# Performance work log

Hardware: AMD Instinct MI355X
Metric: run time of the kernel (lower is better)

Reference implementation:

```python
import jax, jax.numpy as jnp
import numpy as np

L = 64          # chain length
D = 16          # bond dimension
S = 2           # local (spin) dimension
N = 131072      # batch of spin configurations


def setup_inputs() -> dict:
    key = jax.random.key(0)
    k1, k2, k3, k4 = jax.random.split(key, 4)
    scale = 1.0 / np.sqrt(D * S)  # matches init_tensors normal_(0, 1/sqrt(D*S))
    left = jax.random.normal(k1, (1, D, S), dtype=jnp.float32) * scale
    bulk = jax.random.normal(k2, (D, D, S), dtype=jnp.float32) * scale
    right = jax.random.normal(k3, (D, 1, S), dtype=jnp.float32) * scale
    x = jax.random.randint(k4, (N, L), 0, S)
    return {"x": x, "left": left, "bulk": bulk, "right": right}


def reference(x, left, bulk, right):
    # x: (N, L) int spins; amplitude(x) -> (N,)
    n, l = x.shape
    # left (1,D,S): gather left matrix per sample -> (N, D) (row vector, left bond is 1)
    leftT = left[0].T                      # (S, D)
    m0 = leftT[x[:, 0]]                    # (N, D)
    bulkT = jnp.transpose(bulk, (2, 0, 1))  # (S, D, D)
    xs = x[:, 1:l - 1].T                   # (L-2, N) bulk-site spins

    def step(m, s):
        # m: (N, D), bulkT[s]: (N, D, D) -> batched vec-mat product
        return jnp.einsum('nd,nde->ne', m, bulkT[s]), None

    m, _ = jax.lax.scan(step, m0, xs)      # (N, D)
    rightT = jnp.transpose(right, (2, 0, 1))[:, :, 0]  # (S, D)
    a = jnp.einsum('nd,nd->n', m, rightT[x[:, l - 1]])  # (N,)
    return a
```

## Files before the change

### kernel.cpp

```cpp
#include <hip/hip_runtime.h>

#define OFF_V    0u
#define OFF_W    262144u
#define OFF_P    524288u
#define OFF_VA   1048576u
#define OFF_WB   1050624u
#define OFF_PAV  1052672u
#define OFF_PAW  1085440u
#define OFF_PC0  1118208u
#define OFF_PC1  1150976u
#define OFF_PACK 1167360u

__device__ __forceinline__ void rmul16(float* v, const float* B) {
  float nv[16];
#pragma unroll
  for (int e = 0; e < 16; ++e) {
    float a = 0.f;
#pragma unroll
    for (int d = 0; d < 16; ++d) a = fmaf(v[d], B[d * 16 + e], a);
    nv[e] = a;
  }
#pragma unroll
  for (int e = 0; e < 16; ++e) v[e] = nv[e];
}

__device__ __forceinline__ void lmul16(float* v, const float* B) {
  float nv[16];
#pragma unroll
  for (int d = 0; d < 16; ++d) {
    float a = 0.f;
#pragma unroll
    for (int e = 0; e < 16; ++e) a = fmaf(B[d * 16 + e], v[e], a);
    nv[d] = a;
  }
#pragma unroll
  for (int d = 0; d < 16; ++d) v[d] = nv[d];
}

__global__ __launch_bounds__(256) void build_a(const float* __restrict__ left,
                                               const float* __restrict__ bulk,
                                               const float* __restrict__ right,
                                               const int* __restrict__ x,
                                               float* __restrict__ ws) {
  int tid = threadIdx.x;

  if (blockIdx.x >= 29) {
    int lane = tid & 63;
    int wave = tid >> 6;
    unsigned pb = blockIdx.x - 29;
    unsigned seqbase = pb * 256u + wave * 64u;
    const int* __restrict__ xp = x + (size_t)seqbase * 64;
    unsigned long long word = 0ull;
#pragma unroll
    for (int rb = 0; rb < 8; ++rb) {
      int vals[8];
#pragma unroll
      for (int j = 0; j < 8; ++j) vals[j] = xp[(size_t)(rb * 8 + j) * 64 + lane];
#pragma unroll
      for (int j = 0; j < 8; ++j) {
        unsigned long long mm = __ballot(vals[j] & 1);
        if (lane == rb * 8 + j) word = mm;
      }
    }
    reinterpret_cast<unsigned long long*>(ws + OFF_PACK)[seqbase + lane] = word;
    return;
  }

  __shared__ float Bs[2][256];
  __shared__ float Ls[2][16];
  __shared__ float Rs[2][16];
  for (int i = tid; i < 576; i += 256) {
    if (i < 512) Bs[i & 1][i >> 1] = bulk[i];
    else if (i < 544) { int j = i - 512; Ls[j & 1][j >> 1] = left[j]; }
    else              { int j = i - 544; Rs[j & 1][j >> 1] = right[j]; }
  }
  __syncthreads();

  unsigned gid = blockIdx.x * 256 + tid;
  float v[16];
  if (gid < 128) {
    unsigned i = gid;
#pragma unroll
    for (int d = 0; d < 16; ++d) v[d] = Ls[i & 1][d];
    for (int t = 1; t <= 6; ++t) rmul16(v, Bs[(i >> t) & 1]);
#pragma unroll
    for (int d = 0; d < 16; ++d) ws[OFF_VA + i * 16 + d] = v[d];
  } else if (gid < 256) {
    unsigned i = gid - 128;
#pragma unroll
    for (int d = 0; d < 16; ++d) v[d] = Rs[(i >> 6) & 1][d];
    for (int p = 5; p >= 0; --p) lmul16(v, Bs[(i >> p) & 1]);
#pragma unroll
    for (int d = 0; d < 16; ++d) ws[OFF_WB + i * 16 + d] = v[d];
  } else if (gid < 2304) {
    unsigned it = gid - 256, i = it >> 4, col = it & 15;
#pragma unroll
    for (int d = 0; d < 16; ++d) v[d] = Bs[(i >> 6) & 1][d * 16 + col];
    for (int p = 5; p >= 0; --p) lmul16(v, Bs[(i >> p) & 1]);
#pragma unroll
    for (int d = 0; d < 16; ++d) ws[OFF_PAV + i * 256 + d * 16 + col] = v[d];
  } else if (gid < 4352) {
    unsigned it = gid - 2304, i = it >> 4, col = it & 15;
#pragma unroll
    for (int d = 0; d < 16; ++d) v[d] = Bs[(i >> 6) & 1][d * 16 + col];
    for (int p = 5; p >= 0; --p) lmul16(v, Bs[(i >> p) & 1]);
#pragma unroll
    for (int d = 0; d < 16; ++d) ws[OFF_PAW + i * 256 + d * 16 + col] = v[d];
  } else {
    unsigned it = gid - 4352, c = it / 768, r = it - c * 768;
    if (r < 512) {
      unsigned i = r >> 4, col = r & 15;
#pragma unroll
      for (int d = 0; d < 16; ++d) v[d] = Bs[(i >> 4) & 1][d * 16 + col];
      for (int p = 3; p >= 0; --p) lmul16(v, Bs[(i >> p) & 1]);
#pragma unroll
      for (int d = 0; d < 16; ++d) ws[OFF_PC0 + c * 8192 + i * 256 + d * 16 + col] = v[d];
    } else {
      unsigned r2 = r - 512, i = r2 >> 4, col = r2 & 15;
#pragma unroll
      for (int d = 0; d < 16; ++d) v[d] = Bs[(i >> 3) & 1][d * 16 + col];
      for (int p = 2; p >= 0; --p) lmul16(v, Bs[(i >> p) & 1]);
#pragma unroll
      for (int d = 0; d < 16; ++d) ws[OFF_PC1 + c * 4096 + i * 256 + d * 16 + col] = v[d];
    }
  }
}

__global__ __launch_bounds__(256) void build_b(float* __restrict__ ws) {
  unsigned gid = blockIdx.x * 256 + threadIdx.x;
  if (gid < 262144u) {
    unsigned i = gid >> 4, e = gid & 15;
    const float* va = ws + OFF_VA + (i & 127) * 16;
    const float* pm = ws + OFF_PAV + (i >> 7) * 256;
    float a = 0.f;
#pragma unroll
    for (int k = 0; k < 16; ++k) a = fmaf(va[k], pm[k * 16 + e], a);
    ws[OFF_V + (size_t)i * 16 + e] = a;
  } else if (gid < 524288u) {
    unsigned g = gid - 262144u, i = g >> 4, d = g & 15;
    const float* wb = ws + OFF_WB + (i >> 7) * 16;
    const float* pm = ws + OFF_PAW + (i & 127) * 256 + d * 16;
    float a = 0.f;
#pragma unroll
    for (int k = 0; k < 16; ++k) a = fmaf(pm[k], wb[k], a);
    ws[OFF_W + (size_t)i * 16 + d] = a;
  } else {
    unsigned g = gid - 524288u;
    unsigned c = g >> 17, rem = g & 131071u;
    unsigned idx = rem >> 8, d = (rem >> 4) & 15, e = rem & 15;
    const float* p0 = ws + OFF_PC0 + c * 8192 + (idx & 31) * 256 + d * 16;
    const float* p1 = ws + OFF_PC1 + c * 4096 + (idx >> 5) * 256 + e;
    float a = 0.f;
#pragma unroll
    for (int k = 0; k < 16; ++k) a = fmaf(p0[k], p1[k * 16], a);
    ws[OFF_P + ((size_t)c << 17) + (size_t)idx * 256 + d * 16 + e] = a;
  }
}

__global__ __launch_bounds__(256, 4) void mps_main(const float* __restrict__ ws,
                                                   float* __restrict__ out) {
  __shared__ float sm[4][4][16];
  const int tid = threadIdx.x;
  const int lane = tid & 63;
  const int wave = tid >> 6;
  const int grp = lane >> 4;
  const int e = lane & 15;
  const unsigned seqw = blockIdx.x * 16u + wave * 4u;

  unsigned long long bits =
      reinterpret_cast<const unsigned long long*>(ws + OFF_PACK)[seqw + grp];

  const unsigned i0 = (unsigned)(bits & 0x3FFFull);
  const unsigned iw = (unsigned)(bits >> 50);
  unsigned idx0 = (unsigned)((bits >> 14) & 511ull);
  unsigned idx1 = (unsigned)((bits >> 23) & 511ull);
  unsigned idx2 = (unsigned)((bits >> 32) & 511ull);
  unsigned idx3 = (unsigned)((bits >> 41) & 511ull);

  float mv = ws[OFF_V + (size_t)i0 * 16 + e];
  float w  = ws[OFF_W + (size_t)iw * 16 + e];

  const float* __restrict__ P0 = ws + OFF_P;
  float p[4][16];
  {
    const float* pb = P0 + (size_t)idx0 * 256 + e;
#pragma unroll
    for (int d = 0; d < 16; ++d) p[0][d] = pb[d * 16];
  }
  {
    const float* pb = P0 + (1u << 17) + (size_t)idx1 * 256 + e;
#pragma unroll
    for (int d = 0; d < 16; ++d) p[1][d] = pb[d * 16];
  }
  {
    const float* pb = P0 + (2u << 17) + (size_t)idx2 * 256 + e;
#pragma unroll
    for (int d = 0; d < 16; ++d) p[2][d] = pb[d * 16];
  }
  {
    const float* pb = P0 + (3u << 17) + (size_t)idx3 * 256 + e;
#pragma unroll
    for (int d = 0; d < 16; ++d) p[3][d] = pb[d * 16];
  }

#pragma unroll
  for (int ch = 0; ch < 4; ++ch) {
    sm[wave][grp][e] = mv;
    asm volatile("" ::: "memory");
    float4 M0 = *(const float4*)&sm[wave][grp][0];
    float4 M1 = *(const float4*)&sm[wave][grp][4];
    float4 M2 = *(const float4*)&sm[wave][grp][8];
    float4 M3 = *(const float4*)&sm[wave][grp][12];
    asm volatile("" ::: "memory");
    float a0 = M0.x * p[ch][0];
    float a1 = M0.y * p[ch][1];
    float a2 = M0.z * p[ch][2];
    float a3 = M0.w * p[ch][3];
    a0 = fmaf(M1.x, p[ch][4], a0);
    a1 = fmaf(M1.y, p[ch][5], a1);
    a2 = fmaf(M1.z, p[ch][6], a2);
    a3 = fmaf(M1.w, p[ch][7], a3);
    a0 = fmaf(M2.x, p[ch][8], a0);
    a1 = fmaf(M2.y, p[ch][9], a1);
    a2 = fmaf(M2.z, p[ch][10], a2);
    a3 = fmaf(M2.w, p[ch][11], a3);
    a0 = fmaf(M3.x, p[ch][12], a0);
    a1 = fmaf(M3.y, p[ch][13], a1);
    a2 = fmaf(M3.z, p[ch][14], a2);
    a3 = fmaf(M3.w, p[ch][15], a3);
    mv = (a0 + a1) + (a2 + a3);
  }

  float part = mv * w;
  part += __shfl_xor(part, 1, 64);
  part += __shfl_xor(part, 2, 64);
  part += __shfl_xor(part, 4, 64);
  part += __shfl_xor(part, 8, 64);
  if (e == 0) out[seqw + grp] = part;
}

extern "C" void kernel_launch(void* const* d_in, const int* in_sizes, int n_in,
                              void* d_out, int out_size, void* d_ws, size_t ws_size,
                              hipStream_t stream) {
  const int* x = (const int*)d_in[0];
  const float* left = (const float*)d_in[1];
  const float* bulk = (const float*)d_in[2];
  const float* right = (const float*)d_in[3];
  float* out = (float*)d_out;
  float* ws = (float*)d_ws;

  int nseq = in_sizes[0] / 64;

  build_a<<<29 + nseq / 256, 256, 0, stream>>>(left, bulk, right, x, ws);
  build_b<<<4096, 256, 0, stream>>>(ws);
  mps_main<<<nseq / 16, 256, 0, stream>>>(ws, out);
}
```

Baseline: 120.9 us.

## Transpose chunk-product layout for float4 loads and move bit packing to build_b

The spin bit-packing work moves from build_a to build_b, so build_a runs only the 29 small table-building blocks. The chunk-product matrices P are now stored transposed, which lets mps_main fetch each column as four float4 loads instead of sixteen strided scalar loads. The LDS broadcast of the state vector is replaced by wave shuffles. Nontemporal load and store hints are added for the packed bits and the output. The risks are a longer build_b kernel and the cost of the shuffle instructions.

Result: slower. 139.1 us (+15.1%).

```diff
diff --git a/kernel.cpp b/kernel.cpp
--- a/kernel.cpp
+++ b/kernel.cpp
@@ -40,32 +40,8 @@
 __global__ __launch_bounds__(256) void build_a(const float* __restrict__ left,
                                                const float* __restrict__ bulk,
                                                const float* __restrict__ right,
-                                               const int* __restrict__ x,
                                                float* __restrict__ ws) {
   int tid = threadIdx.x;
-
-  if (blockIdx.x >= 29) {
-    int lane = tid & 63;
-    int wave = tid >> 6;
-    unsigned pb = blockIdx.x - 29;
-    unsigned seqbase = pb * 256u + wave * 64u;
-    const int* __restrict__ xp = x + (size_t)seqbase * 64;
-    unsigned long long word = 0ull;
-#pragma unroll
-    for (int rb = 0; rb < 8; ++rb) {
-      int vals[8];
-#pragma unroll
-      for (int j = 0; j < 8; ++j) vals[j] = xp[(size_t)(rb * 8 + j) * 64 + lane];
-#pragma unroll
-      for (int j = 0; j < 8; ++j) {
-        unsigned long long mm = __ballot(vals[j] & 1);
-        if (lane == rb * 8 + j) word = mm;
-      }
-    }
-    reinterpret_cast<unsigned long long*>(ws + OFF_PACK)[seqbase + lane] = word;
-    return;
-  }
-
   __shared__ float Bs[2][256];
   __shared__ float Ls[2][16];
   __shared__ float Rs[2][16];
@@ -126,8 +102,33 @@
   }
 }
 
-__global__ __launch_bounds__(256) void build_b(float* __restrict__ ws) {
-  unsigned gid = blockIdx.x * 256 + threadIdx.x;
+__global__ __launch_bounds__(256) void build_b(const int* __restrict__ x,
+                                               float* __restrict__ ws) {
+  int tid = threadIdx.x;
+
+  if (blockIdx.x >= 4096) {
+    int lane = tid & 63;
+    int wave = tid >> 6;
+    unsigned pb = blockIdx.x - 4096;
+    unsigned seqbase = pb * 256u + wave * 64u;
+    const int* __restrict__ xp = x + (size_t)seqbase * 64;
+    unsigned long long word = 0ull;
+#pragma unroll
+    for (int rb = 0; rb < 8; ++rb) {
+      int vals[8];
+#pragma unroll
+      for (int j = 0; j < 8; ++j) vals[j] = xp[(size_t)(rb * 8 + j) * 64 + lane];
+#pragma unroll
+      for (int j = 0; j < 8; ++j) {
+        unsigned long long mm = __ballot(vals[j] & 1);
+        if (lane == rb * 8 + j) word = mm;
+      }
+    }
+    reinterpret_cast<unsigned long long*>(ws + OFF_PACK)[seqbase + lane] = word;
+    return;
+  }
+
+  unsigned gid = blockIdx.x * 256 + tid;
   if (gid < 262144u) {
     unsigned i = gid >> 4, e = gid & 15;
     const float* va = ws + OFF_VA + (i & 127) * 16;
@@ -147,87 +148,81 @@
   } else {
     unsigned g = gid - 524288u;
     unsigned c = g >> 17, rem = g & 131071u;
-    unsigned idx = rem >> 8, d = (rem >> 4) & 15, e = rem & 15;
-    const float* p0 = ws + OFF_PC0 + c * 8192 + (idx & 31) * 256 + d * 16;
+    unsigned idx = rem >> 8, e = (rem >> 4) & 15, d = rem & 15;
+    const float4* p0 =
+        reinterpret_cast<const float4*>(ws + OFF_PC0 + c * 8192 + (idx & 31) * 256 + d * 16);
     const float* p1 = ws + OFF_PC1 + c * 4096 + (idx >> 5) * 256 + e;
-    float a = 0.f;
-#pragma unroll
-    for (int k = 0; k < 16; ++k) a = fmaf(p0[k], p1[k * 16], a);
-    ws[OFF_P + ((size_t)c << 17) + (size_t)idx * 256 + d * 16 + e] = a;
+    float4 r0 = p0[0], r1 = p0[1], r2 = p0[2], r3 = p0[3];
+    float a;
+    a = r0.x * p1[0];
+    a = fmaf(r0.y, p1[16], a);
+    a = fmaf(r0.z, p1[32], a);
+    a = fmaf(r0.w, p1[48], a);
+    a = fmaf(r1.x, p1[64], a);
+    a = fmaf(r1.y, p1[80], a);
+    a = fmaf(r1.z, p1[96], a);
+    a = fmaf(r1.w, p1[112], a);
+    a = fmaf(r2.x, p1[128], a);
+    a = fmaf(r2.y, p1[144], a);
+    a = fmaf(r2.z, p1[160], a);
+    a = fmaf(r2.w, p1[176], a);
+    a = fmaf(r3.x, p1[192], a);
+    a = fmaf(r3.y, p1[208], a);
+    a = fmaf(r3.z, p1[224], a);
+    a = fmaf(r3.w, p1[240], a);
+    ws[OFF_P + ((size_t)c << 17) + (size_t)idx * 256 + e * 16 + d] = a;
   }
 }
 
 __global__ __launch_bounds__(256, 4) void mps_main(const float* __restrict__ ws,
                                                    float* __restrict__ out) {
-  __shared__ float sm[4][4][16];
   const int tid = threadIdx.x;
   const int lane = tid & 63;
   const int wave = tid >> 6;
   const int grp = lane >> 4;
+  const int grpbase = lane & 48;
   const int e = lane & 15;
   const unsigned seqw = blockIdx.x * 16u + wave * 4u;
 
-  unsigned long long bits =
-      reinterpret_cast<const unsigned long long*>(ws + OFF_PACK)[seqw + grp];
+  unsigned long long bits = __builtin_nontemporal_load(
+      reinterpret_cast<const unsigned long long*>(ws + OFF_PACK) + seqw + grp);
 
   const unsigned i0 = (unsigned)(bits & 0x3FFFull);
   const unsigned iw = (unsigned)(bits >> 50);
-  unsigned idx0 = (unsigned)((bits >> 14) & 511ull);
-  unsigned idx1 = (unsigned)((bits >> 23) & 511ull);
-  unsigned idx2 = (unsigned)((bits >> 32) & 511ull);
-  unsigned idx3 = (unsigned)((bits >> 41) & 511ull);
 
   float mv = ws[OFF_V + (size_t)i0 * 16 + e];
   float w  = ws[OFF_W + (size_t)iw * 16 + e];
 
-  const float* __restrict__ P0 = ws + OFF_P;
-  float p[4][16];
-  {
-    const float* pb = P0 + (size_t)idx0 * 256 + e;
-#pragma unroll
-    for (int d = 0; d < 16; ++d) p[0][d] = pb[d * 16];
-  }
-  {
-    const float* pb = P0 + (1u << 17) + (size_t)idx1 * 256 + e;
-#pragma unroll
-    for (int d = 0; d < 16; ++d) p[1][d] = pb[d * 16];
-  }
-  {
-    const float* pb = P0 + (2u << 17) + (size_t)idx2 * 256 + e;
-#pragma unroll
-    for (int d = 0; d < 16; ++d) p[2][d] = pb[d * 16];
-  }
-  {
-    const float* pb = P0 + (3u << 17) + (size_t)idx3 * 256 + e;
-#pragma unroll
-    for (int d = 0; d < 16; ++d) p[3][d] = pb[d * 16];
-  }
-
+  float4 q[4][4];
 #pragma unroll
   for (int ch = 0; ch < 4; ++ch) {
-    sm[wave][grp][e] = mv;
-    asm volatile("" ::: "memory");
-    float4 M0 = *(const float4*)&sm[wave][grp][0];
-    float4 M1 = *(const float4*)&sm[wave][grp][4];
-    float4 M2 = *(const float4*)&sm[wave][grp][8];
-    float4 M3 = *(const float4*)&sm[wave][grp][12];
-    asm volatile("" ::: "memory");
-    float a0 = M0.x * p[ch][0];
-    float a1 = M0.y * p[ch][1];
-    float a2 = M0.z * p[ch][2];
-    float a3 = M0.w * p[ch][3];
-    a0 = fmaf(M1.x, p[ch][4], a0);
-    a1 = fmaf(M1.y, p[ch][5], a1);
-    a2 = fmaf(M1.z, p[ch][6], a2);
-    a3 = fmaf(M1.w, p[ch][7], a3);
-    a0 = fmaf(M2.x, p[ch][8], a0);
-    a1 = fmaf(M2.y, p[ch][9], a1);
-    a2 = fmaf(M2.z, p[ch][10], a2);
-    a3 = fmaf(M2.w, p[ch][11], a3);
-    a0 = fmaf(M3.x, p[ch][12], a0);
-    a1 = fmaf(M3.y, p[ch][13], a1);
-    a2 = fmaf(M3.z, p[ch][14], a2);
-    a3 = fmaf(M3.w, p[ch][15], a3);
+    unsigned idx = (unsigned)((bits >> (14 + 9 * ch)) & 511ull);
+    const float4* pb = reinterpret_cast<const float4*>(ws + OFF_P + ((size_t)ch << 17)) +
+                       (size_t)idx * 64 + e * 4;
+    q[ch][0] = pb[0];
+    q[ch][1] = pb[1];
+    q[ch][2] = pb[2];
+    q[ch][3] = pb[3];
+  }
+
+#pragma unroll
+  for (int ch = 0; ch < 4; ++ch) {
+    float a0, a1, a2, a3;
+    {
+      float4 qq = q[ch][0];
+      a0 = __shfl(mv, grpbase + 0) * qq.x;
+      a1 = __shfl(mv, grpbase + 1) * qq.y;
+      a2 = __shfl(mv, grpbase + 2) * qq.z;
+      a3 = __shfl(mv, grpbase + 3) * qq.w;
+    }
+#pragma unroll
+    for (int j = 1; j < 4; ++j) {
+      float4 qq = q[ch][j];
+      a0 = fmaf(__shfl(mv, grpbase + j * 4 + 0), qq.x, a0);
+      a1 = fmaf(__shfl(mv, grpbase + j * 4 + 1), qq.y, a1);
+      a2 = fmaf(__shfl(mv, grpbase + j * 4 + 2), qq.z, a2);
+      a3 = fmaf(__shfl(mv, grpbase + j * 4 + 3), qq.w, a3);
+    }
     mv = (a0 + a1) + (a2 + a3);
   }
 
@@ -236,7 +231,7 @@
   part += __shfl_xor(part, 2, 64);
   part += __shfl_xor(part, 4, 64);
   part += __shfl_xor(part, 8, 64);
-  if (e == 0) out[seqw + grp] = part;
+  if (e == 0) __builtin_nontemporal_store(part, out + seqw + grp);
 }
 
 extern "C" void kernel_launch(void* const* d_in, const int* in_sizes, int n_in,
@@ -251,7 +246,7 @@
 
   int nseq = in_sizes[0] / 64;
 
-  build_a<<<29 + nseq / 256, 256, 0, stream>>>(left, bulk, right, x, ws);
-  build_b<<<4096, 256, 0, stream>>>(ws);
+  build_a<<<29, 256, 0, stream>>>(left, bulk, right, ws);
+  build_b<<<4096 + nseq / 256, 256, 0, stream>>>(x, ws);
   mps_main<<<nseq / 16, 256, 0, stream>>>(ws, out);
 }
```
